# Kernel tuning notes

Hardware: AMD Instinct MI355X
Metric: run time of the kernel (lower is better)

## Reference

```python
import jax, jax.numpy as jnp
from jax import lax
import numpy as np

V, E, H, L, B, S, T = 32000, 1024, 1024, 2, 64, 128, 32


def setup_inputs() -> dict:
    key = jax.random.key(0)
    ks = jax.random.split(key, 16)
    s = 0.05
    f = lambda k, shape: (jax.random.normal(k, shape, dtype=jnp.float32) * s)
    return {
        "src": jax.random.randint(ks[0], (B, S), 0, V),
        "src_len": jax.random.randint(ks[1], (B,), 1, S + 1),
        "trg": jax.random.randint(ks[2], (B, T), 0, V),
        "emb": f(ks[3], (V, E)),
        "enc_Wih": f(ks[4], (L, 3 * H, H)),
        "enc_Whh": f(ks[5], (L, 3 * H, H)),
        "enc_bih": f(ks[6], (L, 3 * H)),
        "enc_bhh": f(ks[7], (L, 3 * H)),
        "dec_Wih": f(ks[8], (L, 3 * H, H)),
        "dec_Whh": f(ks[9], (L, 3 * H, H)),
        "dec_bih": f(ks[10], (L, 3 * H)),
        "dec_bhh": f(ks[11], (L, 3 * H)),
        "fc_W": f(ks[12], (V, H)),
        "fc_b": f(ks[13], (V,)),
    }


def _gru_cell(x, h, Wih, Whh, bih, bhh):
    # PyTorch GRU cell math. x:[B,in], h:[B,H]
    gi = x @ Wih.T + bih  # [B,3H]
    gh = h @ Whh.T + bhh  # [B,3H]
    i_r, i_z, i_n = jnp.split(gi, 3, axis=-1)
    h_r, h_z, h_n = jnp.split(gh, 3, axis=-1)
    r = jax.nn.sigmoid(i_r + h_r)
    z = jax.nn.sigmoid(i_z + h_z)
    n = jnp.tanh(i_n + r * h_n)
    return (1.0 - z) * n + z * h


def reference(src, src_len, trg, emb,
              enc_Wih, enc_Whh, enc_bih, enc_bhh,
              dec_Wih, dec_Whh, dec_bih, dec_bhh,
              fc_W, fc_b):
    # ---- Encoder: masked scan reproduces pack_padded_sequence final hidden ----
    xs = emb[src]  # [B,S,E]
    valid = (jnp.arange(S)[None, :] < src_len[:, None]).T  # [S,B]

    def enc_step(h, inputs):
        x_t, v = inputs  # x_t:[B,E], v:[B]
        inp = x_t
        new_h = []
        for l in range(L):
            hn = _gru_cell(inp, h[l], enc_Wih[l], enc_Whh[l], enc_bih[l], enc_bhh[l])
            hn = jnp.where(v[:, None], hn, h[l])
            new_h.append(hn)
            inp = hn
        return jnp.stack(new_h), None

    h0 = jnp.zeros((L, B, H), dtype=emb.dtype)
    hidden, _ = lax.scan(enc_step, h0, (xs.transpose(1, 0, 2), valid))

    def dec_step(carry, _):
        h, tok = carry
        inp = emb[tok]  # [B,E]
        new_h = []
        for l in range(L):
            hn = _gru_cell(inp, h[l], dec_Wih[l], dec_Whh[l], dec_bih[l], dec_bhh[l])
            new_h.append(hn)
            inp = hn
        pred = inp @ fc_W.T + fc_b  # [B,V]
        nxt = jnp.argmax(pred, axis=1)
        return (jnp.stack(new_h), nxt), pred

    (_, _), preds = lax.scan(dec_step, (hidden, trg[:, 0]), None, length=T - 1)
    # outputs[:,0,:] stays zero, as in the torch module
    zeros0 = jnp.zeros((1, B, V), dtype=preds.dtype)
    outputs = jnp.concatenate([zeros0, preds], axis=0).transpose(1, 0, 2)  # [B,T,V]
    return outputs
```

## Files before the change

kernel.cpp:

```cpp
#include <hip/hip_runtime.h>
#include <cstddef>

#define Vv 32000
#define Ee 1024
#define Hh 1024
#define Bb 64
#define Ss 128
#define Tt 32
#define H3 3072
#define KSPLIT 8
#define CH 16

template<bool GATHER>
__global__ __launch_bounds__(256)
void big_gemm(const float* __restrict__ Af,
              const float* __restrict__ emb,
              const int* __restrict__ src,
              const float* __restrict__ W,
              float* __restrict__ C, int m_off)
{
  __shared__ __align__(16) float As[16][64];
  __shared__ __align__(16) float Bs[16][64];
  const int tid = threadIdx.x;
  const int m0 = blockIdx.x * 64;
  const int n0 = blockIdx.y * 64;
  const int lm = tid >> 2;
  const int lk = (tid & 3) << 2;

  const float* arow;
  if (GATHER) {
    int m = m_off + m0 + lm;
    int b = m & (Bb - 1), t = m >> 6;
    arow = emb + (size_t)src[b * Ss + t] * Ee;
  } else {
    arow = Af + (size_t)(m_off + m0 + lm) * 1024;
  }
  const float* wrow = W + (size_t)(n0 + lm) * 1024;

  float acc[4][4];
  #pragma unroll
  for (int i = 0; i < 4; ++i)
    #pragma unroll
    for (int j = 0; j < 4; ++j) acc[i][j] = 0.f;

  const int tm = (tid >> 4) << 2;
  const int tn = (tid & 15) << 2;

  for (int k0 = 0; k0 < 1024; k0 += 16) {
    float4 a = *(const float4*)(arow + k0 + lk);
    As[lk+0][lm] = a.x; As[lk+1][lm] = a.y;
    As[lk+2][lm] = a.z; As[lk+3][lm] = a.w;
    float4 w = *(const float4*)(wrow + k0 + lk);
    Bs[lk+0][lm] = w.x; Bs[lk+1][lm] = w.y;
    Bs[lk+2][lm] = w.z; Bs[lk+3][lm] = w.w;
    __syncthreads();
    #pragma unroll
    for (int kk = 0; kk < 16; ++kk) {
      const float4 a = *(const float4*)&As[kk][tm];
      const float4 b = *(const float4*)&Bs[kk][tn];
      acc[0][0] += a.x*b.x; acc[0][1] += a.x*b.y; acc[0][2] += a.x*b.z; acc[0][3] += a.x*b.w;
      acc[1][0] += a.y*b.x; acc[1][1] += a.y*b.y; acc[1][2] += a.y*b.z; acc[1][3] += a.y*b.w;
      acc[2][0] += a.z*b.x; acc[2][1] += a.z*b.y; acc[2][2] += a.z*b.z; acc[2][3] += a.z*b.w;
      acc[3][0] += a.w*b.x; acc[3][1] += a.w*b.y; acc[3][2] += a.w*b.z; acc[3][3] += a.w*b.w;
    }
    __syncthreads();
  }
  #pragma unroll
  for (int i = 0; i < 4; ++i) {
    float4 v; v.x = acc[i][0]; v.y = acc[i][1]; v.z = acc[i][2]; v.w = acc[i][3];
    *(float4*)(C + (size_t)(m0 + tm + i) * H3 + n0 + tn) = v;
  }
}

template<bool S0_GATHER>
__global__ __launch_bounds__(256)
void small_gemm(const float* __restrict__ A0, const float* __restrict__ gemb,
                const int* __restrict__ rows0,
                const float* __restrict__ W0, float* __restrict__ P0,
                const float* __restrict__ A1, const float* __restrict__ W1,
                float* __restrict__ P1)
{
  __shared__ __align__(16) float As[16][64];
  __shared__ __align__(16) float Bs[16][64];
  const int tid = threadIdx.x;
  const int n0 = blockIdx.x * 64;
  const int kbase = blockIdx.y * 128;
  const int slot = blockIdx.z;
  const float* W = (slot == 0) ? W0 : W1;
  float* dst = ((slot == 0) ? P0 : P1) + (size_t)blockIdx.y * (64 * H3);

  const int lm = tid >> 2;
  const int lk = (tid & 3) << 2;

  const float* arow;
  if (S0_GATHER && (slot == 0)) {
    arow = gemb + (size_t)rows0[lm] * Ee;
  } else {
    const float* Af = (slot == 0) ? A0 : A1;
    arow = Af + (size_t)lm * 1024;
  }
  const float* wrow = W + (size_t)(n0 + lm) * 1024;

  float acc[4][4];
  #pragma unroll
  for (int i = 0; i < 4; ++i)
    #pragma unroll
    for (int j = 0; j < 4; ++j) acc[i][j] = 0.f;

  const int tm = (tid >> 4) << 2;
  const int tn = (tid & 15) << 2;

  for (int k0 = kbase; k0 < kbase + 128; k0 += 16) {
    float4 a = *(const float4*)(arow + k0 + lk);
    As[lk+0][lm] = a.x; As[lk+1][lm] = a.y;
    As[lk+2][lm] = a.z; As[lk+3][lm] = a.w;
    float4 w = *(const float4*)(wrow + k0 + lk);
    Bs[lk+0][lm] = w.x; Bs[lk+1][lm] = w.y;
    Bs[lk+2][lm] = w.z; Bs[lk+3][lm] = w.w;
    __syncthreads();
    #pragma unroll
    for (int kk = 0; kk < 16; ++kk) {
      const float4 a = *(const float4*)&As[kk][tm];
      const float4 b = *(const float4*)&Bs[kk][tn];
      acc[0][0] += a.x*b.x; acc[0][1] += a.x*b.y; acc[0][2] += a.x*b.z; acc[0][3] += a.x*b.w;
      acc[1][0] += a.y*b.x; acc[1][1] += a.y*b.y; acc[1][2] += a.y*b.z; acc[1][3] += a.y*b.w;
      acc[2][0] += a.z*b.x; acc[2][1] += a.z*b.y; acc[2][2] += a.z*b.z; acc[2][3] += a.z*b.w;
      acc[3][0] += a.w*b.x; acc[3][1] += a.w*b.y; acc[3][2] += a.w*b.z; acc[3][3] += a.w*b.w;
    }
    __syncthreads();
  }
  #pragma unroll
  for (int i = 0; i < 4; ++i) {
    float4 v; v.x = acc[i][0]; v.y = acc[i][1]; v.z = acc[i][2]; v.w = acc[i][3];
    *(float4*)(dst + (size_t)(tm + i) * H3 + n0 + tn) = v;
  }
}

__global__ __launch_bounds__(256)
void gru_gates(const float* __restrict__ gi, int ngi,
               const float* __restrict__ gh, int ngh,
               const float* __restrict__ bih, const float* __restrict__ bhh,
               float* __restrict__ h, float* __restrict__ hsave,
               const int* __restrict__ src_len, int t, int use_mask)
{
  int idx = blockIdx.x * 256 + threadIdx.x;
  int b = idx >> 10, j = idx & 1023;
  float sir = 0.f, siz = 0.f, sin_ = 0.f;
  for (int p = 0; p < ngi; ++p) {
    const float* g = gi + (size_t)p * (64 * H3) + (size_t)b * H3 + j;
    sir += g[0]; siz += g[1024]; sin_ += g[2048];
  }
  float shr = 0.f, shz = 0.f, shn = 0.f;
  for (int p = 0; p < ngh; ++p) {
    const float* g = gh + (size_t)p * (64 * H3) + (size_t)b * H3 + j;
    shr += g[0]; shz += g[1024]; shn += g[2048];
  }
  float r = 1.f / (1.f + expf(-(sir + bih[j]        + shr + bhh[j])));
  float z = 1.f / (1.f + expf(-(siz + bih[j + 1024] + shz + bhh[j + 1024])));
  float n = tanhf(sin_ + bih[j + 2048] + r * (shn + bhh[j + 2048]));
  float hp = h[idx];
  float hn = (1.f - z) * n + z * hp;
  if (use_mask && t >= src_len[b]) hn = hp;
  h[idx] = hn;
  if (hsave) hsave[idx] = hn;
}

__global__ __launch_bounds__(256)
void fc_gemm(const float* __restrict__ A, const float* __restrict__ W,
             const float* __restrict__ bias,
             float* __restrict__ out, int t)
{
  __shared__ __align__(16) float As[16][64];
  __shared__ __align__(16) float Bs[16][64];
  const int tid = threadIdx.x;
  const int n0 = blockIdx.x * 64;
  const int lm = tid >> 2;
  const int lk = (tid & 3) << 2;
  const float* arow = A + (size_t)lm * 1024;
  const float* wrow = W + (size_t)(n0 + lm) * 1024;

  float acc[4][4];
  #pragma unroll
  for (int i = 0; i < 4; ++i)
    #pragma unroll
    for (int j = 0; j < 4; ++j) acc[i][j] = 0.f;

  const int tm = (tid >> 4) << 2;
  const int tn = (tid & 15) << 2;

  for (int k0 = 0; k0 < 1024; k0 += 16) {
    float4 a = *(const float4*)(arow + k0 + lk);
    As[lk+0][lm] = a.x; As[lk+1][lm] = a.y;
    As[lk+2][lm] = a.z; As[lk+3][lm] = a.w;
    float4 w = *(const float4*)(wrow + k0 + lk);
    Bs[lk+0][lm] = w.x; Bs[lk+1][lm] = w.y;
    Bs[lk+2][lm] = w.z; Bs[lk+3][lm] = w.w;
    __syncthreads();
    #pragma unroll
    for (int kk = 0; kk < 16; ++kk) {
      const float4 a = *(const float4*)&As[kk][tm];
      const float4 b = *(const float4*)&Bs[kk][tn];
      acc[0][0] += a.x*b.x; acc[0][1] += a.x*b.y; acc[0][2] += a.x*b.z; acc[0][3] += a.x*b.w;
      acc[1][0] += a.y*b.x; acc[1][1] += a.y*b.y; acc[1][2] += a.y*b.z; acc[1][3] += a.y*b.w;
      acc[2][0] += a.z*b.x; acc[2][1] += a.z*b.y; acc[2][2] += a.z*b.z; acc[2][3] += a.z*b.w;
      acc[3][0] += a.w*b.x; acc[3][1] += a.w*b.y; acc[3][2] += a.w*b.z; acc[3][3] += a.w*b.w;
    }
    __syncthreads();
  }
  #pragma unroll
  for (int i = 0; i < 4; ++i) {
    int m = tm + i;
    float4 v;
    v.x = acc[i][0] + bias[n0 + tn + 0];
    v.y = acc[i][1] + bias[n0 + tn + 1];
    v.z = acc[i][2] + bias[n0 + tn + 2];
    v.w = acc[i][3] + bias[n0 + tn + 3];
    *(float4*)(out + (size_t)m * Tt * Vv + (size_t)t * Vv + n0 + tn) = v;
  }
}

__global__ __launch_bounds__(256)
void argmax_k(const float* __restrict__ out, int t, int* __restrict__ tok)
{
  __shared__ float sv[256];
  __shared__ int   si[256];
  const int b = blockIdx.x;
  const int tid = threadIdx.x;
  const float* logits = out + (size_t)b * Tt * Vv + (size_t)t * Vv;
  float best = -3.4e38f; int bi = 0;
  for (int j = tid; j < Vv; j += 256) {
    float v = logits[j];
    if (v > best) { best = v; bi = j; }
  }
  sv[tid] = best; si[tid] = bi;
  __syncthreads();
  for (int s = 128; s > 0; s >>= 1) {
    if (tid < s) {
      if (sv[tid + s] > sv[tid] || (sv[tid + s] == sv[tid] && si[tid + s] < si[tid])) {
        sv[tid] = sv[tid + s]; si[tid] = si[tid + s];
      }
    }
    __syncthreads();
  }
  if (tid == 0) tok[b] = si[0];
}

__global__ void zero_f32(float* __restrict__ p, int n)
{
  int i = blockIdx.x * 256 + threadIdx.x;
  if (i < n) p[i] = 0.f;
}

__global__ void zero_first(float* __restrict__ out)
{
  int i = blockIdx.x * 256 + threadIdx.x;
  if (i < Bb * Vv) {
    int b = i / Vv, v = i - b * Vv;
    out[(size_t)b * Tt * Vv + v] = 0.f;
  }
}

__global__ void tok_init(int* __restrict__ tok, const int* __restrict__ trg)
{
  int i = threadIdx.x;
  if (i < Bb) tok[i] = trg[i * Tt];
}


extern "C" void kernel_launch(void* const* d_in, const int* in_sizes, int n_in,
                              void* d_out, int out_size, void* d_ws, size_t ws_size,
                              hipStream_t stream)
{
  const int*   src     = (const int*)d_in[0];
  const int*   src_len = (const int*)d_in[1];
  const int*   trg     = (const int*)d_in[2];
  const float* emb     = (const float*)d_in[3];
  const float* enc_Wih = (const float*)d_in[4];
  const float* enc_Whh = (const float*)d_in[5];
  const float* enc_bih = (const float*)d_in[6];
  const float* enc_bhh = (const float*)d_in[7];
  const float* dec_Wih = (const float*)d_in[8];
  const float* dec_Whh = (const float*)d_in[9];
  const float* dec_bih = (const float*)d_in[10];
  const float* dec_bhh = (const float*)d_in[11];
  const float* fc_W    = (const float*)d_in[12];
  const float* fc_b    = (const float*)d_in[13];
  float* outp = (float*)d_out;

  float* ws = (float*)d_ws;
  float* parts0  = ws;
  float* parts1  = parts0 + (size_t)KSPLIT * Bb * H3;
  float* h_state = parts1 + (size_t)KSPLIT * Bb * H3;
  int*   tok     = (int*)(h_state + 2 * Bb * Hh);
  float* gi_ch   = (float*)(tok + 64);
  float* h_all   = gi_ch + (size_t)CH * Bb * H3;

  const size_t Wl = (size_t)H3 * Hh;
  float* h0 = h_state;
  float* h1 = h_state + Bb * Hh;

  zero_f32<<<(2 * Bb * Hh + 255) / 256, 256, 0, stream>>>(h_state, 2 * Bb * Hh);

  for (int c = 0; c < Ss; c += CH) {
    big_gemm<true><<<dim3(CH, 48), 256, 0, stream>>>(nullptr, emb, src, enc_Wih,
                                                     gi_ch, c * Bb);
    for (int t = c; t < c + CH; ++t) {
      small_gemm<false><<<dim3(48, KSPLIT, 1), 256, 0, stream>>>(
          h0, nullptr, nullptr, enc_Whh, parts1, nullptr, nullptr, nullptr);
      gru_gates<<<256, 256, 0, stream>>>(gi_ch + (size_t)(t - c) * Bb * H3, 1,
                                         parts1, KSPLIT, enc_bih, enc_bhh, h0,
                                         h_all + (size_t)t * Bb * Hh, src_len, t, 1);
    }
  }
  for (int c = 0; c < Ss; c += CH) {
    big_gemm<false><<<dim3(CH, 48), 256, 0, stream>>>(h_all, nullptr, nullptr,
                                                      enc_Wih + Wl, gi_ch, c * Bb);
    for (int t = c; t < c + CH; ++t) {
      small_gemm<false><<<dim3(48, KSPLIT, 1), 256, 0, stream>>>(
          h1, nullptr, nullptr, enc_Whh + Wl, parts1, nullptr, nullptr, nullptr);
      gru_gates<<<256, 256, 0, stream>>>(gi_ch + (size_t)(t - c) * Bb * H3, 1,
                                         parts1, KSPLIT, enc_bih + H3, enc_bhh + H3, h1,
                                         nullptr, src_len, t, 1);
    }
  }

  zero_first<<<(Bb * Vv + 255) / 256, 256, 0, stream>>>(outp);
  tok_init<<<1, 64, 0, stream>>>(tok, trg);

  for (int t = 1; t < Tt; ++t) {
    small_gemm<true><<<dim3(48, KSPLIT, 2), 256, 0, stream>>>(
        nullptr, emb, tok, dec_Wih, parts0, h0, dec_Whh, parts1);
    gru_gates<<<256, 256, 0, stream>>>(parts0, KSPLIT, parts1, KSPLIT,
                                       dec_bih, dec_bhh, h0, nullptr, nullptr, 0, 0);
    small_gemm<false><<<dim3(48, KSPLIT, 2), 256, 0, stream>>>(
        h0, nullptr, nullptr, dec_Wih + Wl, parts0, h1, dec_Whh + Wl, parts1);
    gru_gates<<<256, 256, 0, stream>>>(parts0, KSPLIT, parts1, KSPLIT,
                                       dec_bih + H3, dec_bhh + H3, h1, nullptr, nullptr, 0, 0);
    fc_gemm<<<dim3(Vv / 64), 256, 0, stream>>>(h1, fc_W, fc_b, outp, t);
    argmax_k<<<64, 256, 0, stream>>>(outp, t, tok);
  }
}
```

Measured before the change: 11.58 ms.

## Wavefront-pipeline the two encoder GRU layers into one fused per-step loop

Replaces the two sequential encoder layer passes with a single wavefront loop. At step t, layer 0 runs time t while layer 1 runs time t-1. Each step issues one fused GEMM launch covering h0·Whh0, h0·Wih1 and h1·Whh1, and one combined gates launch. This cuts the number of per-step launches and the h_all round trip, and gives each launch more parallel blocks. The trade-off is that layer 1's input projection is now computed per step with split-K partial sums instead of as a batched big GEMM, and gates2 must read h0 before it is overwritten.

```diff
diff --git a/kernel.cpp b/kernel.cpp
--- a/kernel.cpp
+++ b/kernel.cpp
@@ -11,42 +11,22 @@
 #define KSPLIT 8
 #define CH 16
 
-template<bool GATHER>
-__global__ __launch_bounds__(256)
-void big_gemm(const float* __restrict__ Af,
-              const float* __restrict__ emb,
-              const int* __restrict__ src,
-              const float* __restrict__ W,
-              float* __restrict__ C, int m_off)
-{
-  __shared__ __align__(16) float As[16][64];
-  __shared__ __align__(16) float Bs[16][64];
-  const int tid = threadIdx.x;
-  const int m0 = blockIdx.x * 64;
-  const int n0 = blockIdx.y * 64;
+__device__ __forceinline__
+void mm_tile(const float* __restrict__ arow, const float* __restrict__ wrow,
+             float (&As)[16][64], float (&Bs)[16][64], float (&acc)[4][4],
+             int kbeg, int kend)
+{
+  const int tid = threadIdx.x;
+  const int lk = (tid & 3) << 2;
   const int lm = tid >> 2;
-  const int lk = (tid & 3) << 2;
-
-  const float* arow;
-  if (GATHER) {
-    int m = m_off + m0 + lm;
-    int b = m & (Bb - 1), t = m >> 6;
-    arow = emb + (size_t)src[b * Ss + t] * Ee;
-  } else {
-    arow = Af + (size_t)(m_off + m0 + lm) * 1024;
-  }
-  const float* wrow = W + (size_t)(n0 + lm) * 1024;
-
-  float acc[4][4];
+  const int tm = (tid >> 4) << 2;
+  const int tn = (tid & 15) << 2;
   #pragma unroll
   for (int i = 0; i < 4; ++i)
     #pragma unroll
     for (int j = 0; j < 4; ++j) acc[i][j] = 0.f;
 
-  const int tm = (tid >> 4) << 2;
-  const int tn = (tid & 15) << 2;
-
-  for (int k0 = 0; k0 < 1024; k0 += 16) {
+  for (int k0 = kbeg; k0 < kend; k0 += 16) {
     float4 a = *(const float4*)(arow + k0 + lk);
     As[lk+0][lm] = a.x; As[lk+1][lm] = a.y;
     As[lk+2][lm] = a.z; As[lk+3][lm] = a.w;
@@ -56,94 +36,37 @@
     __syncthreads();
     #pragma unroll
     for (int kk = 0; kk < 16; ++kk) {
-      const float4 a = *(const float4*)&As[kk][tm];
-      const float4 b = *(const float4*)&Bs[kk][tn];
-      acc[0][0] += a.x*b.x; acc[0][1] += a.x*b.y; acc[0][2] += a.x*b.z; acc[0][3] += a.x*b.w;
-      acc[1][0] += a.y*b.x; acc[1][1] += a.y*b.y; acc[1][2] += a.y*b.z; acc[1][3] += a.y*b.w;
-      acc[2][0] += a.z*b.x; acc[2][1] += a.z*b.y; acc[2][2] += a.z*b.z; acc[2][3] += a.z*b.w;
-      acc[3][0] += a.w*b.x; acc[3][1] += a.w*b.y; acc[3][2] += a.w*b.z; acc[3][3] += a.w*b.w;
+      const float4 av = *(const float4*)&As[kk][tm];
+      const float4 bv = *(const float4*)&Bs[kk][tn];
+      acc[0][0] += av.x*bv.x; acc[0][1] += av.x*bv.y; acc[0][2] += av.x*bv.z; acc[0][3] += av.x*bv.w;
+      acc[1][0] += av.y*bv.x; acc[1][1] += av.y*bv.y; acc[1][2] += av.y*bv.z; acc[1][3] += av.y*bv.w;
+      acc[2][0] += av.z*bv.x; acc[2][1] += av.z*bv.y; acc[2][2] += av.z*bv.z; acc[2][3] += av.z*bv.w;
+      acc[3][0] += av.w*bv.x; acc[3][1] += av.w*bv.y; acc[3][2] += av.w*bv.z; acc[3][3] += av.w*bv.w;
     }
     __syncthreads();
   }
+}
+
+__device__ __forceinline__
+void store_tile(float* __restrict__ dst, const float (&acc)[4][4])
+{
+  const int tid = threadIdx.x;
+  const int tm = (tid >> 4) << 2;
+  const int tn = (tid & 15) << 2;
   #pragma unroll
   for (int i = 0; i < 4; ++i) {
     float4 v; v.x = acc[i][0]; v.y = acc[i][1]; v.z = acc[i][2]; v.w = acc[i][3];
-    *(float4*)(C + (size_t)(m0 + tm + i) * H3 + n0 + tn) = v;
-  }
-}
-
-template<bool S0_GATHER>
-__global__ __launch_bounds__(256)
-void small_gemm(const float* __restrict__ A0, const float* __restrict__ gemb,
-                const int* __restrict__ rows0,
-                const float* __restrict__ W0, float* __restrict__ P0,
-                const float* __restrict__ A1, const float* __restrict__ W1,
-                float* __restrict__ P1)
-{
-  __shared__ __align__(16) float As[16][64];
-  __shared__ __align__(16) float Bs[16][64];
-  const int tid = threadIdx.x;
-  const int n0 = blockIdx.x * 64;
-  const int kbase = blockIdx.y * 128;
-  const int slot = blockIdx.z;
-  const float* W = (slot == 0) ? W0 : W1;
-  float* dst = ((slot == 0) ? P0 : P1) + (size_t)blockIdx.y * (64 * H3);
-
-  const int lm = tid >> 2;
-  const int lk = (tid & 3) << 2;
-
-  const float* arow;
-  if (S0_GATHER && (slot == 0)) {
-    arow = gemb + (size_t)rows0[lm] * Ee;
-  } else {
-    const float* Af = (slot == 0) ? A0 : A1;
-    arow = Af + (size_t)lm * 1024;
-  }
-  const float* wrow = W + (size_t)(n0 + lm) * 1024;
-
-  float acc[4][4];
-  #pragma unroll
-  for (int i = 0; i < 4; ++i)
-    #pragma unroll
-    for (int j = 0; j < 4; ++j) acc[i][j] = 0.f;
-
-  const int tm = (tid >> 4) << 2;
-  const int tn = (tid & 15) << 2;
-
-  for (int k0 = kbase; k0 < kbase + 128; k0 += 16) {
-    float4 a = *(const float4*)(arow + k0 + lk);
-    As[lk+0][lm] = a.x; As[lk+1][lm] = a.y;
-    As[lk+2][lm] = a.z; As[lk+3][lm] = a.w;
-    float4 w = *(const float4*)(wrow + k0 + lk);
-    Bs[lk+0][lm] = w.x; Bs[lk+1][lm] = w.y;
-    Bs[lk+2][lm] = w.z; Bs[lk+3][lm] = w.w;
-    __syncthreads();
-    #pragma unroll
-    for (int kk = 0; kk < 16; ++kk) {
-      const float4 a = *(const float4*)&As[kk][tm];
-      const float4 b = *(const float4*)&Bs[kk][tn];
-      acc[0][0] += a.x*b.x; acc[0][1] += a.x*b.y; acc[0][2] += a.x*b.z; acc[0][3] += a.x*b.w;
-      acc[1][0] += a.y*b.x; acc[1][1] += a.y*b.y; acc[1][2] += a.y*b.z; acc[1][3] += a.y*b.w;
-      acc[2][0] += a.z*b.x; acc[2][1] += a.z*b.y; acc[2][2] += a.z*b.z; acc[2][3] += a.z*b.w;
-      acc[3][0] += a.w*b.x; acc[3][1] += a.w*b.y; acc[3][2] += a.w*b.z; acc[3][3] += a.w*b.w;
-    }
-    __syncthreads();
-  }
-  #pragma unroll
-  for (int i = 0; i < 4; ++i) {
-    float4 v; v.x = acc[i][0]; v.y = acc[i][1]; v.z = acc[i][2]; v.w = acc[i][3];
-    *(float4*)(dst + (size_t)(tm + i) * H3 + n0 + tn) = v;
-  }
-}
-
-__global__ __launch_bounds__(256)
-void gru_gates(const float* __restrict__ gi, int ngi,
-               const float* __restrict__ gh, int ngh,
-               const float* __restrict__ bih, const float* __restrict__ bhh,
-               float* __restrict__ h, float* __restrict__ hsave,
-               const int* __restrict__ src_len, int t, int use_mask)
-{
-  int idx = blockIdx.x * 256 + threadIdx.x;
+    *(float4*)(dst + (size_t)(tm + i) * H3 + tn) = v;
+  }
+}
+
+__device__ __forceinline__
+void gates_op(int idx, const float* __restrict__ gi, int ngi,
+              const float* __restrict__ gh, int ngh,
+              const float* __restrict__ bih, const float* __restrict__ bhh,
+              float* __restrict__ h, float* __restrict__ hsave,
+              const int* __restrict__ src_len, int t, int use_mask)
+{
   int b = idx >> 10, j = idx & 1023;
   float sir = 0.f, siz = 0.f, sin_ = 0.f;
   for (int p = 0; p < ngi; ++p) {
@@ -166,6 +89,125 @@
 }
 
 __global__ __launch_bounds__(256)
+void big_gemm_gather(const float* __restrict__ emb,
+                     const int* __restrict__ src,
+                     const float* __restrict__ W,
+                     float* __restrict__ C, int m_off)
+{
+  __shared__ __align__(16) float As[16][64];
+  __shared__ __align__(16) float Bs[16][64];
+  const int tid = threadIdx.x;
+  const int m0 = blockIdx.x * 64;
+  const int n0 = blockIdx.y * 64;
+  const int lm = tid >> 2;
+
+  int m = m_off + m0 + lm;
+  int b = m & (Bb - 1), t = m >> 6;
+  const float* arow = emb + (size_t)src[b * Ss + t] * Ee;
+  const float* wrow = W + (size_t)(n0 + lm) * 1024;
+  float acc[4][4];
+  mm_tile(arow, wrow, As, Bs, acc, 0, 1024);
+  store_tile(C + (size_t)m0 * H3 + n0, acc);
+}
+
+__global__ __launch_bounds__(256)
+void fat_enc(const float* __restrict__ h0, const float* __restrict__ h1,
+             const float* __restrict__ Whh0, const float* __restrict__ Wih1,
+             const float* __restrict__ Whh1,
+             float* __restrict__ pgh0, float* __restrict__ pgi1,
+             float* __restrict__ pgh1, int has0)
+{
+  __shared__ __align__(16) float As[16][64];
+  __shared__ __align__(16) float Bs[16][64];
+  const int lm = threadIdx.x >> 2;
+  int r = blockIdx.x;
+
+  if (has0 && r < 384) {
+    const int ntile = r % 48;
+    const int ks = r / 48;
+    const float* arow = h0 + (size_t)lm * 1024;
+    const float* wrow = Whh0 + (size_t)(ntile * 64 + lm) * 1024;
+    float acc[4][4];
+    mm_tile(arow, wrow, As, Bs, acc, ks * 128, ks * 128 + 128);
+    store_tile(pgh0 + (size_t)ks * (64 * H3) + ntile * 64, acc);
+    return;
+  }
+  r -= has0 ? 384 : 0;
+  const int which = r / 384;
+  const int rr = r - which * 384;
+  const int ntile = rr % 48;
+  const int ks = rr / 48;
+  const float* arow = (which == 0 ? h0 : h1) + (size_t)lm * 1024;
+  const float* wrow = (which == 0 ? Wih1 : Whh1) + (size_t)(ntile * 64 + lm) * 1024;
+  float acc[4][4];
+  mm_tile(arow, wrow, As, Bs, acc, ks * 128, ks * 128 + 128);
+  store_tile((which == 0 ? pgi1 : pgh1) + (size_t)ks * (64 * H3) + ntile * 64, acc);
+}
+
+__global__ __launch_bounds__(256)
+void gates2(const float* __restrict__ gi0, const float* __restrict__ pgh0,
+            const float* __restrict__ bih0, const float* __restrict__ bhh0,
+            float* __restrict__ h0,
+            const float* __restrict__ pgi1, const float* __restrict__ pgh1,
+            const float* __restrict__ bih1, const float* __restrict__ bhh1,
+            float* __restrict__ h1,
+            const int* __restrict__ src_len, int t, int has0, int has1)
+{
+  const int blk = blockIdx.x;
+  if (blk < 256) {
+    if (!has0) return;
+    const int idx = blk * 256 + threadIdx.x;
+    gates_op(idx, gi0, 1, pgh0, KSPLIT, bih0, bhh0, h0, nullptr, src_len, t, 1);
+  } else {
+    if (!has1) return;
+    const int idx = (blk - 256) * 256 + threadIdx.x;
+    gates_op(idx, pgi1, KSPLIT, pgh1, KSPLIT, bih1, bhh1, h1, nullptr, src_len, t - 1, 1);
+  }
+}
+
+template<bool S0_GATHER>
+__global__ __launch_bounds__(256)
+void small_gemm(const float* __restrict__ A0, const float* __restrict__ gemb,
+                const int* __restrict__ rows0,
+                const float* __restrict__ W0, float* __restrict__ P0,
+                const float* __restrict__ A1, const float* __restrict__ W1,
+                float* __restrict__ P1)
+{
+  __shared__ __align__(16) float As[16][64];
+  __shared__ __align__(16) float Bs[16][64];
+  const int tid = threadIdx.x;
+  const int n0 = blockIdx.x * 64;
+  const int kbase = blockIdx.y * 128;
+  const int slot = blockIdx.z;
+  const float* W = (slot == 0) ? W0 : W1;
+  float* dst = ((slot == 0) ? P0 : P1) + (size_t)blockIdx.y * (64 * H3);
+  const int lm = tid >> 2;
+
+  const float* arow;
+  if (S0_GATHER && (slot == 0)) {
+    arow = gemb + (size_t)rows0[lm] * Ee;
+  } else {
+    const float* Af = (slot == 0) ? A0 : A1;
+    arow = Af + (size_t)lm * 1024;
+  }
+  const float* wrow = W + (size_t)(n0 + lm) * 1024;
+  float acc[4][4];
+  mm_tile(arow, wrow, As, Bs, acc, kbase, kbase + 128);
+  store_tile(dst + n0, acc);
+}
+
+__global__ __launch_bounds__(256)
+void gru_gates(const float* __restrict__ gi, int ngi,
+               const float* __restrict__ gh, int ngh,
+               const float* __restrict__ bih, const float* __restrict__ bhh,
+               float* __restrict__ h, float* __restrict__ hsave,
+               const int* __restrict__ src_len, int t, int use_mask)
+{
+  int idx = blockIdx.x * 256 + threadIdx.x;
+  gates_op(idx, gi, ngi, gh, ngh, bih, bhh, h, hsave, src_len, t, use_mask);
+}
+
+__global__ __launch_bounds__(256)
 void fc_gemm(const float* __restrict__ A, const float* __restrict__ W,
              const float* __restrict__ bias,
              float* __restrict__ out, int t)
@@ -175,38 +217,12 @@
   const int tid = threadIdx.x;
   const int n0 = blockIdx.x * 64;
   const int lm = tid >> 2;
-  const int lk = (tid & 3) << 2;
   const float* arow = A + (size_t)lm * 1024;
   const float* wrow = W + (size_t)(n0 + lm) * 1024;
-
   float acc[4][4];
-  #pragma unroll
-  for (int i = 0; i < 4; ++i)
-    #pragma unroll
-    for (int j = 0; j < 4; ++j) acc[i][j] = 0.f;
-
+  mm_tile(arow, wrow, As, Bs, acc, 0, 1024);
   const int tm = (tid >> 4) << 2;
   const int tn = (tid & 15) << 2;
-
-  for (int k0 = 0; k0 < 1024; k0 += 16) {
-    float4 a = *(const float4*)(arow + k0 + lk);
-    As[lk+0][lm] = a.x; As[lk+1][lm] = a.y;
-    As[lk+2][lm] = a.z; As[lk+3][lm] = a.w;
-    float4 w = *(const float4*)(wrow + k0 + lk);
-    Bs[lk+0][lm] = w.x; Bs[lk+1][lm] = w.y;
-    Bs[lk+2][lm] = w.z; Bs[lk+3][lm] = w.w;
-    __syncthreads();
-    #pragma unroll
-    for (int kk = 0; kk < 16; ++kk) {
-      const float4 a = *(const float4*)&As[kk][tm];
-      const float4 b = *(const float4*)&Bs[kk][tn];
-      acc[0][0] += a.x*b.x; acc[0][1] += a.x*b.y; acc[0][2] += a.x*b.z; acc[0][3] += a.x*b.w;
-      acc[1][0] += a.y*b.x; acc[1][1] += a.y*b.y; acc[1][2] += a.y*b.z; acc[1][3] += a.y*b.w;
-      acc[2][0] += a.z*b.x; acc[2][1] += a.z*b.y; acc[2][2] += a.z*b.z; acc[2][3] += a.z*b.w;
-      acc[3][0] += a.w*b.x; acc[3][1] += a.w*b.y; acc[3][2] += a.w*b.z; acc[3][3] += a.w*b.w;
-    }
-    __syncthreads();
-  }
   #pragma unroll
   for (int i = 0; i < 4; ++i) {
     int m = tm + i;
@@ -288,53 +304,49 @@
   float* outp = (float*)d_out;
 
   float* ws = (float*)d_ws;
-  float* parts0  = ws;
-  float* parts1  = parts0 + (size_t)KSPLIT * Bb * H3;
-  float* h_state = parts1 + (size_t)KSPLIT * Bb * H3;
+  const size_t PART = (size_t)KSPLIT * Bb * H3;
+  float* pgh0    = ws;
+  float* pgi1    = pgh0 + PART;
+  float* pgh1    = pgi1 + PART;
+  float* h_state = pgh1 + PART;
   int*   tok     = (int*)(h_state + 2 * Bb * Hh);
   float* gi_ch   = (float*)(tok + 64);
-  float* h_all   = gi_ch + (size_t)CH * Bb * H3;
 
   const size_t Wl = (size_t)H3 * Hh;
   float* h0 = h_state;
   float* h1 = h_state + Bb * Hh;
 
   zero_f32<<<(2 * Bb * Hh + 255) / 256, 256, 0, stream>>>(h_state, 2 * Bb * Hh);
-
-  for (int c = 0; c < Ss; c += CH) {
-    big_gemm<true><<<dim3(CH, 48), 256, 0, stream>>>(nullptr, emb, src, enc_Wih,
-                                                     gi_ch, c * Bb);
-    for (int t = c; t < c + CH; ++t) {
-      small_gemm<false><<<dim3(48, KSPLIT, 1), 256, 0, stream>>>(
-          h0, nullptr, nullptr, enc_Whh, parts1, nullptr, nullptr, nullptr);
-      gru_gates<<<256, 256, 0, stream>>>(gi_ch + (size_t)(t - c) * Bb * H3, 1,
-                                         parts1, KSPLIT, enc_bih, enc_bhh, h0,
-                                         h_all + (size_t)t * Bb * Hh, src_len, t, 1);
-    }
-  }
-  for (int c = 0; c < Ss; c += CH) {
-    big_gemm<false><<<dim3(CH, 48), 256, 0, stream>>>(h_all, nullptr, nullptr,
-                                                      enc_Wih + Wl, gi_ch, c * Bb);
-    for (int t = c; t < c + CH; ++t) {
-      small_gemm<false><<<dim3(48, KSPLIT, 1), 256, 0, stream>>>(
-          h1, nullptr, nullptr, enc_Whh + Wl, parts1, nullptr, nullptr, nullptr);
-      gru_gates<<<256, 256, 0, stream>>>(gi_ch + (size_t)(t - c) * Bb * H3, 1,
-                                         parts1, KSPLIT, enc_bih + H3, enc_bhh + H3, h1,
-                                         nullptr, src_len, t, 1);
-    }
-  }
-
   zero_first<<<(Bb * Vv + 255) / 256, 256, 0, stream>>>(outp);
   tok_init<<<1, 64, 0, stream>>>(tok, trg);
 
+  for (int t = 0; t <= Ss; ++t) {
+    const int has0 = (t < Ss) ? 1 : 0;
+    const int has1 = (t >= 1) ? 1 : 0;
+
+    if (has0 && (t & (CH - 1)) == 0) {
+      big_gemm_gather<<<dim3(CH, 48), 256, 0, stream>>>(emb, src, enc_Wih,
+                                                        gi_ch, t * Bb);
+    }
+
+    const int slot = t & (CH - 1);
+    const int ntasks = (has0 ? 384 : 0) + (has1 ? 768 : 0);
+    fat_enc<<<ntasks, 256, 0, stream>>>(h0, h1, enc_Whh, enc_Wih + Wl,
+                                        enc_Whh + Wl, pgh0, pgi1, pgh1, has0);
+    gates2<<<512, 256, 0, stream>>>(gi_ch + (size_t)slot * (64 * H3),
+                                    pgh0, enc_bih, enc_bhh, h0,
+                                    pgi1, pgh1, enc_bih + H3, enc_bhh + H3, h1,
+                                    src_len, t, has0, has1);
+  }
+
   for (int t = 1; t < Tt; ++t) {
     small_gemm<true><<<dim3(48, KSPLIT, 2), 256, 0, stream>>>(
-        nullptr, emb, tok, dec_Wih, parts0, h0, dec_Whh, parts1);
-    gru_gates<<<256, 256, 0, stream>>>(parts0, KSPLIT, parts1, KSPLIT,
+        nullptr, emb, tok, dec_Wih, pgh0, h0, dec_Whh, pgi1);
+    gru_gates<<<256, 256, 0, stream>>>(pgh0, KSPLIT, pgi1, KSPLIT,
                                        dec_bih, dec_bhh, h0, nullptr, nullptr, 0, 0);
     small_gemm<false><<<dim3(48, KSPLIT, 2), 256, 0, stream>>>(
-        h0, nullptr, nullptr, dec_Wih + Wl, parts0, h1, dec_Whh + Wl, parts1);
-    gru_gates<<<256, 256, 0, stream>>>(parts0, KSPLIT, parts1, KSPLIT,
+        h0, nullptr, nullptr, dec_Wih + Wl, pgh0, h1, dec_Whh + Wl, pgi1);
+    gru_gates<<<256, 256, 0, stream>>>(pgh0, KSPLIT, pgi1, KSPLIT,
                                        dec_bih + H3, dec_bhh + H3, h1, nullptr, nullptr, 0, 0);
     fc_gemm<<<dim3(Vv / 64), 256, 0, stream>>>(h1, fc_W, fc_b, outp, t);
     argmax_k<<<64, 256, 0, stream>>>(outp, t, tok);
```

New measurement: 9.900 ms. -14.5%, faster.
